# Optimization experiments

Hardware: AMD Instinct MI355X
Metric: run time of the kernel (lower is better)

The kernel has to match this reference:

```python
import jax, jax.numpy as jnp
import numpy as np

B, N, C = 4, 2048, 384
H = 6
D = C // H
HID = int(C * 4.0)
EPS = 1e-5


def setup_inputs() -> dict:
    key = jax.random.key(0)
    ks = jax.random.split(key, 12)
    s = lambda fan_in: 1.0 / np.sqrt(fan_in)
    return {
        "x": jax.random.normal(ks[0], (B, N, C), dtype=jnp.float32),
        "ln1_g": jnp.ones((C,), jnp.float32),
        "ln1_b": jnp.zeros((C,), jnp.float32),
        "w_qkv": jax.random.uniform(ks[1], (C, 3 * C), jnp.float32, -s(C), s(C)),
        "w_proj": jax.random.uniform(ks[2], (C, C), jnp.float32, -s(C), s(C)),
        "b_proj": jax.random.uniform(ks[3], (C,), jnp.float32, -s(C), s(C)),
        "ln2_g": jnp.ones((C,), jnp.float32),
        "ln2_b": jnp.zeros((C,), jnp.float32),
        "w_fc1": jax.random.uniform(ks[4], (C, HID), jnp.float32, -s(C), s(C)),
        "b_fc1": jax.random.uniform(ks[5], (HID,), jnp.float32, -s(C), s(C)),
        "w_fc2": jax.random.uniform(ks[6], (HID, C), jnp.float32, -s(HID), s(HID)),
        "b_fc2": jax.random.uniform(ks[7], (C,), jnp.float32, -s(HID), s(HID)),
    }


def _layernorm(x, g, b):
    mu = jnp.mean(x, axis=-1, keepdims=True)
    var = jnp.mean(jnp.square(x - mu), axis=-1, keepdims=True)
    return (x - mu) * jax.lax.rsqrt(var + EPS) * g + b


def reference(x, ln1_g, ln1_b, w_qkv, w_proj, b_proj, ln2_g, ln2_b, w_fc1, b_fc1, w_fc2, b_fc2):
    # --- attention branch (pre-norm) ---
    h = _layernorm(x, ln1_g, ln1_b)                       # [B,N,C]
    qkv = (h @ w_qkv).reshape(B, N, 3, H, D)
    q = jnp.transpose(qkv[:, :, 0], (0, 2, 1, 3))          # [B,H,N,D]
    k = jnp.transpose(qkv[:, :, 1], (0, 2, 1, 3))
    v = jnp.transpose(qkv[:, :, 2], (0, 2, 1, 3))
    scale = D ** -0.5
    attn = jnp.einsum("bhnd,bhmd->bhnm", q, k) * scale     # [B,H,N,N]
    attn = jax.nn.softmax(attn, axis=-1)
    o = jnp.einsum("bhnm,bhmd->bhnd", attn, v)             # [B,H,N,D]
    o = jnp.transpose(o, (0, 2, 1, 3)).reshape(B, N, C)
    x = x + (o @ w_proj + b_proj)
    # --- MLP branch (pre-norm) ---
    h2 = _layernorm(x, ln2_g, ln2_b)
    m = jax.nn.gelu(h2 @ w_fc1 + b_fc1, approximate=False)  # torch nn.GELU = exact erf
    x = x + (m @ w_fc2 + b_fc2)
    return x
```

## Files before the change

kernel.cpp:

```cpp
#include <hip/hip_runtime.h>

typedef __bf16 bf16x8 __attribute__((ext_vector_type(8)));
typedef float f32x4 __attribute__((ext_vector_type(4)));
typedef float f32x16 __attribute__((ext_vector_type(16)));
typedef unsigned short u16;
typedef unsigned int u32;
typedef unsigned long long u64;

#define BB 4
#define NNCTX 2048
#define CCH 384
#define NHEAD 6
#define DHEAD 64
#define HIDDIM 1536

__device__ __forceinline__ u16 f2bf(float f){
  u32 u = __builtin_bit_cast(u32, f);
  u = u + 0x7fffu + ((u >> 16) & 1u);
  return (u16)(u >> 16);
}
__device__ __forceinline__ float bf2f(u16 h){
  u32 u = ((u32)h) << 16;
  return __builtin_bit_cast(float, u);
}

union U8 { uint4 u; u16 s[8]; bf16x8 v; };
union F8 { u32 w[4]; bf16x8 v; };

__device__ __forceinline__ void gl_lds16(const u16* g, u16* l){
  __builtin_amdgcn_global_load_lds((const __attribute__((address_space(1))) u32*)g,
                                   (__attribute__((address_space(3))) u32*)l, 16, 0, 0);
}

__global__ __launch_bounds__(256) void cast_tr(const float* __restrict__ w0, const float* __restrict__ w1,
    const float* __restrict__ w2, const float* __restrict__ w3,
    u16* __restrict__ o0, u16* __restrict__ o1, u16* __restrict__ o2, u16* __restrict__ o3){
  __shared__ float S[64][65];
  int idx = blockIdx.x;
  const float* src; u16* dst; int K, N, kt, nt;
  if (idx < 108){ src = w0; dst = o0; K = 384; N = 1152; kt = idx / 18; nt = idx % 18; }
  else if (idx < 144){ idx -= 108; src = w1; dst = o1; K = 384; N = 384; kt = idx / 6; nt = idx % 6; }
  else if (idx < 288){ idx -= 144; src = w2; dst = o2; K = 384; N = 1536; kt = idx / 24; nt = idx % 24; }
  else { idx -= 288; src = w3; dst = o3; K = 1536; N = 384; kt = idx / 6; nt = idx % 6; }
  int t = threadIdx.x;
  int r4 = t >> 6, c = t & 63;
  int k0 = kt * 64, n0 = nt * 64;
  #pragma unroll
  for (int i = 0; i < 16; i++){
    int row = i * 4 + r4;
    S[row][c] = src[(size_t)(k0 + row) * N + n0 + c];
  }
  __syncthreads();
  #pragma unroll
  for (int i = 0; i < 16; i++){
    int row = i * 4 + r4;
    dst[(size_t)(n0 + row) * K + k0 + c] = f2bf(S[c][row]);
  }
}

__global__ __launch_bounds__(128) void ln_kernel(const float* __restrict__ x, const float* __restrict__ g,
                                                 const float* __restrict__ bb, u16* __restrict__ out){
  int row = blockIdx.x, t = threadIdx.x;
  const float* xr = x + (size_t)row * CCH;
  float v0 = xr[t], v1 = xr[t + 128], v2 = xr[t + 256];
  float s = v0 + v1 + v2;
  float q = v0 * v0 + v1 * v1 + v2 * v2;
  #pragma unroll
  for (int o = 32; o; o >>= 1){ s += __shfl_down(s, o); q += __shfl_down(q, o); }
  __shared__ float sh[4];
  if ((t & 63) == 0){ int w = t >> 6; sh[w * 2] = s; sh[w * 2 + 1] = q; }
  __syncthreads();
  float sum = sh[0] + sh[2], ssq = sh[1] + sh[3];
  float mu = sum * (1.0f / 384.0f);
  float rstd = rsqrtf(ssq * (1.0f / 384.0f) - mu * mu + 1e-5f);
  size_t base = (size_t)row * CCH;
  out[base + t]       = f2bf((v0 - mu) * rstd * g[t]       + bb[t]);
  out[base + t + 128] = f2bf((v1 - mu) * rstd * g[t + 128] + bb[t + 128]);
  out[base + t + 256] = f2bf((v2 - mu) * rstd * g[t + 256] + bb[t + 256]);
}

template<int EPI>
__global__ __launch_bounds__(256, 4) void gemm_gl(const u16* __restrict__ A, const u16* __restrict__ Bt,
    int K, int Nn, u16* __restrict__ outb, const float* __restrict__ bias)
{
  __shared__ u16 L[16384];
  int t = threadIdx.x;
  int bm = blockIdx.y * 128, bn = blockIdx.x * 128;
  int l = t & 63, w = t >> 6;
  int wm = (w >> 1) * 64, wn = (w & 1) * 64;
  int lr = l & 15, lg = l >> 4;
  f32x4 acc[4][4] = {};
  int grow = l >> 3, gcol = (l & 7) * 8;
  auto STAGE = [&](int k0){
    #pragma unroll
    for (int j = 0; j < 4; j++){
      int c = w * 4 + j;
      const u16* ga = &A[(size_t)(bm + c * 8 + grow) * K + k0 + gcol];
      const u16* gb = &Bt[(size_t)(bn + c * 8 + grow) * K + k0 + gcol];
      gl_lds16(ga, &L[c * 512]);
      gl_lds16(gb, &L[8192 + c * 512]);
    }
  };
  auto COMPUTE = [&](){
    #pragma unroll
    for (int ks = 0; ks < 2; ks++){
      int kb = ks * 32 + lg * 8;
      bf16x8 af[4], bf[4];
      #pragma unroll
      for (int mi = 0; mi < 4; mi++) af[mi] = *(const bf16x8*)&L[(wm + mi * 16 + lr) * 64 + kb];
      #pragma unroll
      for (int ni = 0; ni < 4; ni++) bf[ni] = *(const bf16x8*)&L[8192 + (wn + ni * 16 + lr) * 64 + kb];
      #pragma unroll
      for (int mi = 0; mi < 4; mi++)
        #pragma unroll
        for (int ni = 0; ni < 4; ni++)
          acc[mi][ni] = __builtin_amdgcn_mfma_f32_16x16x32_bf16(af[mi], bf[ni], acc[mi][ni], 0, 0, 0);
    }
  };
  int nk = K >> 6;
  for (int ki = 0; ki < nk; ki++){
    if (ki) __syncthreads();
    STAGE(ki << 6);
    __syncthreads();
    COMPUTE();
  }
  __syncthreads();
  #pragma unroll
  for (int mi = 0; mi < 4; mi++)
  #pragma unroll
  for (int ni = 0; ni < 4; ni++)
  #pragma unroll
  for (int r = 0; r < 4; r++){
    int row = wm + mi * 16 + lg * 4 + r;
    int col = wn + ni * 16 + lr;
    float v = acc[mi][ni][r];
    if (EPI == 2){
      v += bias[bn + col];
      v = 0.5f * v * (1.0f + erff(v * 0.70710678118f));
    }
    L[row * 128 + col] = f2bf(v);
  }
  __syncthreads();
  {
    int row = t >> 1, colh = (t & 1) * 64;
    const uint4* src = (const uint4*)&L[row * 128 + colh];
    uint4* dst = (uint4*)(outb + (size_t)(bm + row) * Nn + bn + colh);
    #pragma unroll
    for (int i = 0; i < 8; i++) dst[i] = src[i];
  }
}

template<int EPI, int DBUF>
__global__ __launch_bounds__(256) void gemm_bf16(const u16* __restrict__ A, const u16* __restrict__ Bt,
    int K, int Nn, u16* __restrict__ outb, const float* __restrict__ bias,
    const float* __restrict__ resid, float* __restrict__ outf)
{
  __shared__ u16 As[DBUF + 1][64][68];
  __shared__ u16 Bs[DBUF + 1][64][68];
  int t = threadIdx.x;
  int bm = blockIdx.y * 64, bn = blockIdx.x * 64;
  int l = t & 63, w = t >> 6;
  int wm = (w >> 1) * 32, wn = (w & 1) * 32;
  f32x4 acc[2][2] = {};
  int ar0 = t >> 3, ac0 = (t & 7) * 8;
  uint4 la0, la1, lb0, lb1;
  auto LOADG = [&](int k0){
    la0 = *(const uint4*)&A[(size_t)(bm + ar0) * K + k0 + ac0];
    la1 = *(const uint4*)&A[(size_t)(bm + ar0 + 32) * K + k0 + ac0];
    lb0 = *(const uint4*)&Bt[(size_t)(bn + ar0) * K + k0 + ac0];
    lb1 = *(const uint4*)&Bt[(size_t)(bn + ar0 + 32) * K + k0 + ac0];
  };
  auto WRITEL = [&](int bf){
    *(uint4*)&As[bf][ar0][ac0]      = la0;
    *(uint4*)&As[bf][ar0 + 32][ac0] = la1;
    *(uint4*)&Bs[bf][ar0][ac0]      = lb0;
    *(uint4*)&Bs[bf][ar0 + 32][ac0] = lb1;
  };
  auto COMPUTE = [&](int bf){
    #pragma unroll
    for (int ks = 0; ks < 2; ks++){
      int kb = ks * 32 + (l >> 4) * 8;
      bf16x8 a0  = *(const bf16x8*)&As[bf][wm + (l & 15)][kb];
      bf16x8 a1  = *(const bf16x8*)&As[bf][wm + 16 + (l & 15)][kb];
      bf16x8 bb0 = *(const bf16x8*)&Bs[bf][wn + (l & 15)][kb];
      bf16x8 bb1 = *(const bf16x8*)&Bs[bf][wn + 16 + (l & 15)][kb];
      acc[0][0] = __builtin_amdgcn_mfma_f32_16x16x32_bf16(a0, bb0, acc[0][0], 0, 0, 0);
      acc[0][1] = __builtin_amdgcn_mfma_f32_16x16x32_bf16(a0, bb1, acc[0][1], 0, 0, 0);
      acc[1][0] = __builtin_amdgcn_mfma_f32_16x16x32_bf16(a1, bb0, acc[1][0], 0, 0, 0);
      acc[1][1] = __builtin_amdgcn_mfma_f32_16x16x32_bf16(a1, bb1, acc[1][1], 0, 0, 0);
    }
  };
  if constexpr (DBUF){
    int nk = K >> 6;
    LOADG(0);
    WRITEL(0);
    __syncthreads();
    for (int ki = 0; ki < nk; ki++){
      int cur = ki & 1;
      if (ki + 1 < nk) LOADG((ki + 1) << 6);
      COMPUTE(cur);
      if (ki + 1 < nk) WRITEL(cur ^ 1);
      __syncthreads();
    }
  } else {
    for (int k0 = 0; k0 < K; k0 += 64){
      __syncthreads();
      LOADG(k0);
      WRITEL(0);
      __syncthreads();
      COMPUTE(0);
    }
  }
  if constexpr (EPI == 1){
    #pragma unroll
    for (int mi = 0; mi < 2; mi++)
    #pragma unroll
    for (int ni = 0; ni < 2; ni++)
    #pragma unroll
    for (int r = 0; r < 4; r++){
      int row = bm + wm + mi * 16 + ((l >> 4) << 2) + r;
      int col = bn + wn + ni * 16 + (l & 15);
      size_t idx = (size_t)row * Nn + col;
      outf[idx] = resid[idx] + acc[mi][ni][r] + bias[col];
    }
  } else {
    __syncthreads();
    u16 (*CS)[68] = As[0];
    #pragma unroll
    for (int mi = 0; mi < 2; mi++)
    #pragma unroll
    for (int ni = 0; ni < 2; ni++)
    #pragma unroll
    for (int r = 0; r < 4; r++){
      int row = wm + mi * 16 + ((l >> 4) << 2) + r;
      int col = wn + ni * 16 + (l & 15);
      float v = acc[mi][ni][r];
      if (EPI == 2){
        v += bias[bn + col];
        v = 0.5f * v * (1.0f + erff(v * 0.70710678118f));
      }
      CS[row][col] = f2bf(v);
    }
    __syncthreads();
    int row = t >> 2, c0 = (t & 3) * 16;
    uint4 v0 = *(const uint4*)&CS[row][c0];
    uint4 v1 = *(const uint4*)&CS[row][c0 + 8];
    u16* op = outb + (size_t)(bm + row) * Nn + bn + c0;
    *(uint4*)op       = v0;
    *(uint4*)(op + 8) = v1;
  }
}

#define PVSTEP(O0, O1, O2, O3, SX, BASE)                                         \
  {                                                                              \
    float p0 = __builtin_exp2f(SX[BASE + 0] - m_q);                              \
    float p1 = __builtin_exp2f(SX[BASE + 1] - m_q);                              \
    float p2 = __builtin_exp2f(SX[BASE + 2] - m_q);                              \
    float p3 = __builtin_exp2f(SX[BASE + 3] - m_q);                              \
    float p4 = __builtin_exp2f(SX[BASE + 4] - m_q);                              \
    float p5 = __builtin_exp2f(SX[BASE + 5] - m_q);                              \
    float p6 = __builtin_exp2f(SX[BASE + 6] - m_q);                              \
    float p7 = __builtin_exp2f(SX[BASE + 7] - m_q);                              \
    u32 wa0, wa1, wb0, wb1;                                                      \
    asm("v_cvt_pk_bf16_f32 %0, %1, %2" : "=v"(wa0) : "v"(p0), "v"(p1));          \
    asm("v_cvt_pk_bf16_f32 %0, %1, %2" : "=v"(wa1) : "v"(p2), "v"(p3));          \
    asm("v_cvt_pk_bf16_f32 %0, %1, %2" : "=v"(wb0) : "v"(p4), "v"(p5));          \
    asm("v_cvt_pk_bf16_f32 %0, %1, %2" : "=v"(wb1) : "v"(p6), "v"(p7));          \
    asm("v_permlane32_swap_b32 %0, %1" : "+v"(wa0), "+v"(wb0));                  \
    asm("v_permlane32_swap_b32 %0, %1" : "+v"(wa1), "+v"(wb1));                  \
    F8 pa; pa.w[0] = wa0; pa.w[1] = wa1; pa.w[2] = wb0; pa.w[3] = wb1;           \
    u64 ta, tb, tc, td;                                                          \
    asm volatile("ds_read_b64_tr_b16 %0, %4 offset:" #O0 "\n\t"                  \
                 "ds_read_b64_tr_b16 %1, %4 offset:" #O1 "\n\t"                  \
                 "ds_read_b64_tr_b16 %2, %4 offset:" #O2 "\n\t"                  \
                 "ds_read_b64_tr_b16 %3, %4 offset:" #O3 "\n\t"                  \
                 "s_waitcnt lgkmcnt(0)"                                          \
                 : "=&v"(ta), "=&v"(tb), "=&v"(tc), "=&v"(td)                    \
                 : "v"(vtr));                                                    \
    __builtin_amdgcn_sched_barrier(0);                                           \
    F8 f0, f1;                                                                   \
    f0.w[0] = (u32)ta; f0.w[1] = (u32)(ta >> 32);                                \
    f0.w[2] = (u32)tb; f0.w[3] = (u32)(tb >> 32);                                \
    f1.w[0] = (u32)tc; f1.w[1] = (u32)(tc >> 32);                                \
    f1.w[2] = (u32)td; f1.w[3] = (u32)(td >> 32);                                \
    l_acc = __builtin_amdgcn_mfma_f32_32x32x16_bf16(pa.v, onesf, l_acc, 0, 0, 0);\
    o_0 = __builtin_amdgcn_mfma_f32_32x32x16_bf16(pa.v, f0.v, o_0, 0, 0, 0);     \
    o_1 = __builtin_amdgcn_mfma_f32_32x32x16_bf16(pa.v, f1.v, o_1, 0, 0, 0);     \
  }

__global__ __launch_bounds__(256, 3) void attn_mfma(const u16* __restrict__ qkv,
    u16* __restrict__ o0buf, u16* __restrict__ o1buf, float2* __restrict__ mlbuf){
  __shared__ u16 Ks[64][68];
  __shared__ __attribute__((aligned(128))) u16 Vs[4096];
  int t = threadIdx.x;
  int w = t >> 6, l = t & 63;
  int c31 = l & 31, hi = l >> 5, hi8 = hi * 8;
  int id = blockIdx.x;
  int xcd = id & 7, slot = id >> 3;
  int qb = slot & 15;
  int group = (slot >> 4) * 8 + xcd;
  int bh = group % (BB * NHEAD);
  int sp = group / (BB * NHEAD);
  int b = bh / NHEAD, h = bh % NHEAD;
  int q0 = qb * 128;

  const float QS = 0.1803368801111716f;
  bf16x8 qf[4];
  {
    const u16* qp = qkv + (size_t)(b * NNCTX + q0 + w * 32 + c31) * 1152 + h * 64 + hi8;
    #pragma unroll
    for (int c = 0; c < 4; c++){
      U8 r; r.u = *(const uint4*)(qp + c * 16);
      #pragma unroll
      for (int j = 0; j < 8; j++) r.s[j] = f2bf(bf2f(r.s[j]) * QS);
      qf[c] = r.v;
    }
  }
  bf16x8 onesf;
  {
    U8 r;
    #pragma unroll
    for (int j = 0; j < 8; j++) r.s[j] = 0x3F80;
    onesf = r.v;
  }
  f32x16 o_0 = {}, o_1 = {};
  f32x16 l_acc = {};
  float m_q = -3.4e38f;

  const size_t kvrow = (size_t)(b * NNCTX) * 1152 + h * 64;
  int kkey = t >> 2, kdp = (t & 3) * 16;
  int vkey = t & 63, vdblk = w * 16;
  int voff = (vkey >> 2) * 256 + w * 64 + (vkey & 3) * 16;
  int lg = l >> 4, lr16 = l & 15;
  u32 vtr = (u32)(uintptr_t)(&Vs[0]) + (u32)((lg >> 1) * 1024 + (lg & 1) * 128 + lr16 * 8);

  uint4 kra, krb, vra, vrb;
  auto LOADT = [&](int kt){
    const u16* kp = qkv + kvrow + (size_t)(kt * 64 + kkey) * 1152 + 384 + kdp;
    kra = *(const uint4*)kp;
    krb = *(const uint4*)(kp + 8);
    const u16* vp = qkv + kvrow + (size_t)(kt * 64 + vkey) * 1152 + 768 + vdblk;
    vra = *(const uint4*)vp;
    vrb = *(const uint4*)(vp + 8);
  };
  auto WRITET = [&](){
    *(uint4*)&Ks[kkey][kdp]     = kra;
    *(uint4*)&Ks[kkey][kdp + 8] = krb;
    *(uint4*)&Vs[voff]     = vra;
    *(uint4*)&Vs[voff + 8] = vrb;
  };

  int ktbeg = sp * 16, ktend = ktbeg + 16;
  LOADT(ktbeg);
  WRITET();
  __syncthreads();

  for (int kt = ktbeg; kt < ktend; kt++){
    if (kt + 1 < ktend) LOADT(kt + 1);

    f32x16 s0 = {}, s1 = {};
    #pragma unroll
    for (int c = 0; c < 4; c++){
      bf16x8 kf0 = *(const bf16x8*)&Ks[c31][c * 16 + hi8];
      bf16x8 kf1 = *(const bf16x8*)&Ks[32 + c31][c * 16 + hi8];
      s0 = __builtin_amdgcn_mfma_f32_32x32x16_bf16(kf0, qf[c], s0, 0, 0, 0);
      s1 = __builtin_amdgcn_mfma_f32_32x32x16_bf16(kf1, qf[c], s1, 0, 0, 0);
    }
    float px = fmaxf(s0[0], s0[1]);
    #pragma unroll
    for (int r = 2; r < 16; r++) px = fmaxf(px, s0[r]);
    #pragma unroll
    for (int r = 0; r < 16; r++) px = fmaxf(px, s1[r]);
    px = fmaxf(px, __shfl_xor(px, 32));
    if (!__all(px <= m_q + 8.f)){
      float mn = fmaxf(m_q, px);
      float a = __builtin_exp2f(m_q - mn);
      m_q = mn;
      #pragma unroll
      for (int r = 0; r < 16; r++){
        int cr = (r & 3) + 8 * (r >> 2) + 4 * hi;
        float ar = __shfl(a, cr);
        o_0[r] *= ar; o_1[r] *= ar; l_acc[r] *= ar;
      }
    }
    PVSTEP(0, 512, 256, 768, s0, 0)
    PVSTEP(2048, 2560, 2304, 2816, s0, 8)
    PVSTEP(4096, 4608, 4352, 4864, s1, 0)
    PVSTEP(6144, 6656, 6400, 6912, s1, 8)

    __syncthreads();
    if (kt + 1 < ktend) WRITET();
    __syncthreads();
  }
  u16* obuf = sp ? o1buf : o0buf;
  #pragma unroll
  for (int r = 0; r < 16; r++){
    int cr = (r & 3) + 8 * (r >> 2) + 4 * hi;
    float mr = __shfl(m_q, cr);
    int n = q0 + w * 32 + cr;
    size_t row = (size_t)(b * NNCTX + n);
    u16* op = obuf + row * CCH + h * 64;
    op[c31]      = f2bf(o_0[r]);
    op[32 + c31] = f2bf(o_1[r]);
    if (c31 == 0)
      mlbuf[((size_t)(sp * BB * NHEAD + bh)) * NNCTX + n] = make_float2(mr, l_acc[r]);
  }
}

__global__ __launch_bounds__(128) void attn_combine(const u16* __restrict__ o0, const u16* __restrict__ o1,
    const float2* __restrict__ ml, u16* __restrict__ obuf){
  __shared__ float sc0[NHEAD], sc1[NHEAD];
  int row = blockIdx.x;
  int b = row >> 11, n = row & 2047;
  int t = threadIdx.x;
  if (t < NHEAD){
    float2 a = ml[(size_t)(b * NHEAD + t) * NNCTX + n];
    float2 c = ml[(size_t)(BB * NHEAD + b * NHEAD + t) * NNCTX + n];
    float M = fmaxf(a.x, c.x);
    float e0 = exp2f(a.x - M), e1 = exp2f(c.x - M);
    float inv = 1.0f / (a.y * e0 + c.y * e1);
    sc0[t] = e0 * inv; sc1[t] = e1 * inv;
  }
  __syncthreads();
  size_t base = (size_t)row * CCH;
  #pragma unroll
  for (int i = 0; i < 3; i++){
    int c = t + i * 128;
    int h = c >> 6;
    float v = bf2f(o0[base + c]) * sc0[h] + bf2f(o1[base + c]) * sc1[h];
    obuf[base + c] = f2bf(v);
  }
}

extern "C" void kernel_launch(void* const* d_in, const int* in_sizes, int n_in,
                              void* d_out, int out_size, void* d_ws, size_t ws_size,
                              hipStream_t stream){
  const float* x      = (const float*)d_in[0];
  const float* ln1_g  = (const float*)d_in[1];
  const float* ln1_b  = (const float*)d_in[2];
  const float* w_qkv  = (const float*)d_in[3];
  const float* w_proj = (const float*)d_in[4];
  const float* b_proj = (const float*)d_in[5];
  const float* ln2_g  = (const float*)d_in[6];
  const float* ln2_b  = (const float*)d_in[7];
  const float* w_fc1  = (const float*)d_in[8];
  const float* b_fc1  = (const float*)d_in[9];
  const float* w_fc2  = (const float*)d_in[10];
  const float* b_fc2  = (const float*)d_in[11];
  float* out = (float*)d_out;

  u16* ws = (u16*)d_ws;
  u16* wqkv_bf  = ws;
  u16* wproj_bf = wqkv_bf + 442368;
  u16* wfc1_bf  = wproj_bf + 147456;
  u16* wfc2_bf  = wfc1_bf + 589824;
  u16* h_bf     = wfc2_bf + 589824;
  u16* qkv_bf   = h_bf + 3145728;
  u16* o_bf     = qkv_bf + 9437184;
  u16* opart1   = o_bf + 3145728;
  float2* mlbuf = (float2*)(opart1 + 3145728);
  u16* opart0   = h_bf;
  u16* m_bf     = qkv_bf;

  cast_tr<<<432, 256, 0, stream>>>(w_qkv, w_proj, w_fc1, w_fc2, wqkv_bf, wproj_bf, wfc1_bf, wfc2_bf);

  ln_kernel<<<8192, 128, 0, stream>>>(x, ln1_g, ln1_b, h_bf);
  gemm_gl<0><<<dim3(9, 64), 256, 0, stream>>>(h_bf, wqkv_bf, 384, 1152, qkv_bf, nullptr);
  attn_mfma<<<dim3(768), 256, 0, stream>>>(qkv_bf, opart0, opart1, mlbuf);
  attn_combine<<<8192, 128, 0, stream>>>(opart0, opart1, mlbuf, o_bf);
  gemm_bf16<1, 1><<<dim3(6, 128), 256, 0, stream>>>(o_bf, wproj_bf, 384, 384, nullptr, b_proj, x, out);
  ln_kernel<<<8192, 128, 0, stream>>>(out, ln2_g, ln2_b, h_bf);
  gemm_gl<2><<<dim3(12, 64), 256, 0, stream>>>(h_bf, wfc1_bf, 384, 1536, m_bf, b_fc1);
  gemm_bf16<1, 1><<<dim3(6, 128), 256, 0, stream>>>(m_bf, wfc2_bf, 1536, 384, nullptr, b_fc2, out, out);
}
```

Before: 162.5 us.

## Double-buffer 128x128 GEMM with XOR-swizzled LDS and vectorize attention combine

The 128x128 GEMM used for QKV and FC1 now double-buffers its LDS tiles, issuing the next K-tile's global-to-LDS loads before computing the current one. It also XOR-swizzles the column layout to avoid LDS bank conflicts. This doubles shared memory and lowers the occupancy hint from 4 to 2 blocks per CU. The attention combine kernel is rewritten to process 8 bf16 values per thread with vector loads and to write in place into opart0, which removes a separate output buffer.

```diff
diff --git a/kernel.cpp b/kernel.cpp
--- a/kernel.cpp
+++ b/kernel.cpp
@@ -80,51 +80,58 @@
 }
 
 template<int EPI>
-__global__ __launch_bounds__(256, 4) void gemm_gl(const u16* __restrict__ A, const u16* __restrict__ Bt,
+__global__ __launch_bounds__(256, 2) void gemm128(const u16* __restrict__ A, const u16* __restrict__ Bt,
     int K, int Nn, u16* __restrict__ outb, const float* __restrict__ bias)
 {
-  __shared__ u16 L[16384];
+  __shared__ u16 L[32768];
   int t = threadIdx.x;
   int bm = blockIdx.y * 128, bn = blockIdx.x * 128;
   int l = t & 63, w = t >> 6;
   int wm = (w >> 1) * 64, wn = (w & 1) * 64;
   int lr = l & 15, lg = l >> 4;
   f32x4 acc[4][4] = {};
-  int grow = l >> 3, gcol = (l & 7) * 8;
-  auto STAGE = [&](int k0){
-    #pragma unroll
-    for (int j = 0; j < 4; j++){
-      int c = w * 4 + j;
-      const u16* ga = &A[(size_t)(bm + c * 8 + grow) * K + k0 + gcol];
-      const u16* gb = &Bt[(size_t)(bn + c * 8 + grow) * K + k0 + gcol];
-      gl_lds16(ga, &L[c * 512]);
-      gl_lds16(gb, &L[8192 + c * 512]);
-    }
-  };
-  auto COMPUTE = [&](){
+  auto STAGE = [&](int bf, int k0){
+    #pragma unroll
+    for (int i = 0; i < 4; i++){
+      int ci = t + i * 256;
+      int row = ci >> 3;
+      int col = (ci & 7) * 8;
+      int gcol = col ^ ((row & 7) << 3);
+      gl_lds16(&A[(size_t)(bm + row) * K + k0 + gcol],  &L[bf * 16384 + ci * 8]);
+      gl_lds16(&Bt[(size_t)(bn + row) * K + k0 + gcol], &L[bf * 16384 + 8192 + ci * 8]);
+    }
+  };
+  auto COMPUTE = [&](int bf){
     #pragma unroll
     for (int ks = 0; ks < 2; ks++){
       int kb = ks * 32 + lg * 8;
-      bf16x8 af[4], bf[4];
+      bf16x8 af[4], bfr[4];
       #pragma unroll
-      for (int mi = 0; mi < 4; mi++) af[mi] = *(const bf16x8*)&L[(wm + mi * 16 + lr) * 64 + kb];
+      for (int mi = 0; mi < 4; mi++){
+        int R = wm + mi * 16 + lr;
+        af[mi] = *(const bf16x8*)&L[bf * 16384 + R * 64 + (kb ^ ((R & 7) << 3))];
+      }
       #pragma unroll
-      for (int ni = 0; ni < 4; ni++) bf[ni] = *(const bf16x8*)&L[8192 + (wn + ni * 16 + lr) * 64 + kb];
+      for (int ni = 0; ni < 4; ni++){
+        int R = wn + ni * 16 + lr;
+        bfr[ni] = *(const bf16x8*)&L[bf * 16384 + 8192 + R * 64 + (kb ^ ((R & 7) << 3))];
+      }
       #pragma unroll
       for (int mi = 0; mi < 4; mi++)
         #pragma unroll
         for (int ni = 0; ni < 4; ni++)
-          acc[mi][ni] = __builtin_amdgcn_mfma_f32_16x16x32_bf16(af[mi], bf[ni], acc[mi][ni], 0, 0, 0);
+          acc[mi][ni] = __builtin_amdgcn_mfma_f32_16x16x32_bf16(af[mi], bfr[ni], acc[mi][ni], 0, 0, 0);
     }
   };
   int nk = K >> 6;
+  STAGE(0, 0);
+  __syncthreads();
   for (int ki = 0; ki < nk; ki++){
-    if (ki) __syncthreads();
-    STAGE(ki << 6);
-    __syncthreads();
-    COMPUTE();
-  }
-  __syncthreads();
+    int cur = ki & 1;
+    if (ki + 1 < nk) STAGE(cur ^ 1, (ki + 1) << 6);
+    COMPUTE(cur);
+    __syncthreads();
+  }
   #pragma unroll
   for (int mi = 0; mi < 4; mi++)
   #pragma unroll
@@ -407,29 +414,26 @@
   }
 }
 
-__global__ __launch_bounds__(128) void attn_combine(const u16* __restrict__ o0, const u16* __restrict__ o1,
-    const float2* __restrict__ ml, u16* __restrict__ obuf){
-  __shared__ float sc0[NHEAD], sc1[NHEAD];
-  int row = blockIdx.x;
+__global__ __launch_bounds__(256) void attn_combine(u16* __restrict__ o0, const u16* __restrict__ o1,
+    const float2* __restrict__ ml){
+  int g = blockIdx.x * 256 + threadIdx.x;
+  int row = g / 48, c8 = g - row * 48;
+  int head = c8 >> 3;
   int b = row >> 11, n = row & 2047;
-  int t = threadIdx.x;
-  if (t < NHEAD){
-    float2 a = ml[(size_t)(b * NHEAD + t) * NNCTX + n];
-    float2 c = ml[(size_t)(BB * NHEAD + b * NHEAD + t) * NNCTX + n];
-    float M = fmaxf(a.x, c.x);
-    float e0 = exp2f(a.x - M), e1 = exp2f(c.x - M);
-    float inv = 1.0f / (a.y * e0 + c.y * e1);
-    sc0[t] = e0 * inv; sc1[t] = e1 * inv;
-  }
-  __syncthreads();
-  size_t base = (size_t)row * CCH;
-  #pragma unroll
-  for (int i = 0; i < 3; i++){
-    int c = t + i * 128;
-    int h = c >> 6;
-    float v = bf2f(o0[base + c]) * sc0[h] + bf2f(o1[base + c]) * sc1[h];
-    obuf[base + c] = f2bf(v);
-  }
+  int bh = b * NHEAD + head;
+  float2 a = ml[(size_t)bh * NNCTX + n];
+  float2 c = ml[(size_t)(BB * NHEAD + bh) * NNCTX + n];
+  float M = fmaxf(a.x, c.x);
+  float e0 = exp2f(a.x - M), e1 = exp2f(c.x - M);
+  float inv = 1.0f / (a.y * e0 + c.y * e1);
+  float s0 = e0 * inv, s1 = e1 * inv;
+  size_t idx = (size_t)row * CCH + c8 * 8;
+  U8 x0, x1, o;
+  x0.u = *(const uint4*)(o0 + idx);
+  x1.u = *(const uint4*)(o1 + idx);
+  #pragma unroll
+  for (int j = 0; j < 8; j++) o.s[j] = f2bf(bf2f(x0.s[j]) * s0 + bf2f(x1.s[j]) * s1);
+  *(uint4*)(o0 + idx) = o.u;
 }
 
 extern "C" void kernel_launch(void* const* d_in, const int* in_sizes, int n_in,
@@ -456,8 +460,7 @@
   u16* wfc2_bf  = wfc1_bf + 589824;
   u16* h_bf     = wfc2_bf + 589824;
   u16* qkv_bf   = h_bf + 3145728;
-  u16* o_bf     = qkv_bf + 9437184;
-  u16* opart1   = o_bf + 3145728;
+  u16* opart1   = qkv_bf + 9437184;
   float2* mlbuf = (float2*)(opart1 + 3145728);
   u16* opart0   = h_bf;
   u16* m_bf     = qkv_bf;
@@ -465,11 +468,11 @@
   cast_tr<<<432, 256, 0, stream>>>(w_qkv, w_proj, w_fc1, w_fc2, wqkv_bf, wproj_bf, wfc1_bf, wfc2_bf);
 
   ln_kernel<<<8192, 128, 0, stream>>>(x, ln1_g, ln1_b, h_bf);
-  gemm_gl<0><<<dim3(9, 64), 256, 0, stream>>>(h_bf, wqkv_bf, 384, 1152, qkv_bf, nullptr);
+  gemm128<0><<<dim3(9, 64), 256, 0, stream>>>(h_bf, wqkv_bf, 384, 1152, qkv_bf, nullptr);
   attn_mfma<<<dim3(768), 256, 0, stream>>>(qkv_bf, opart0, opart1, mlbuf);
-  attn_combine<<<8192, 128, 0, stream>>>(opart0, opart1, mlbuf, o_bf);
-  gemm_bf16<1, 1><<<dim3(6, 128), 256, 0, stream>>>(o_bf, wproj_bf, 384, 384, nullptr, b_proj, x, out);
+  attn_combine<<<1536, 256, 0, stream>>>(opart0, opart1, mlbuf);
+  gemm_bf16<1, 1><<<dim3(6, 128), 256, 0, stream>>>(opart0, wproj_bf, 384, 384, nullptr, b_proj, x, out);
   ln_kernel<<<8192, 128, 0, stream>>>(out, ln2_g, ln2_b, h_bf);
-  gemm_gl<2><<<dim3(12, 64), 256, 0, stream>>>(h_bf, wfc1_bf, 384, 1536, m_bf, b_fc1);
+  gemm128<2><<<dim3(12, 64), 256, 0, stream>>>(h_bf, wfc1_bf, 384, 1536, m_bf, b_fc1);
   gemm_bf16<1, 1><<<dim3(6, 128), 256, 0, stream>>>(m_bf, wfc2_bf, 1536, 384, nullptr, b_fc2, out, out);
 }
```

Measured after the change: 167.5 us. +3.1%, slower.
